# Performance work log

Hardware: AMD Instinct MI355X
Metric: run time of the kernel (lower is better)

Reference implementation:

```python
import jax, jax.numpy as jnp
import numpy as np

CODEBOOK = 512
EMB_DIM = 64
COMMITMENT_COST = 0.25


def setup_inputs() -> dict:
    key = jax.random.key(0)
    k1, k2 = jax.random.split(key)
    inputs = jax.random.normal(k1, (32, EMB_DIM, 64, 64), dtype=jnp.float32)
    # nn.Embedding weight initialized uniform(-1/code_book_dim, 1/code_book_dim)
    embedding = jax.random.uniform(
        k2, (CODEBOOK, EMB_DIM), dtype=jnp.float32,
        minval=-1.0 / CODEBOOK, maxval=1.0 / CODEBOOK)
    return {"inputs": inputs, "embedding": embedding}


def reference(inputs, embedding):
    B, C, H, W = inputs.shape          # C == embedding_dim
    D = embedding.shape[1]
    x = jnp.transpose(inputs, (0, 2, 3, 1))      # [B,H,W,D] (permute(0,2,3,1))
    flat = x.reshape(-1, D)                       # [N,D]
    x2 = jnp.sum(flat * flat, axis=1, keepdims=True)          # [N,1]
    e2 = jnp.sum(embedding * embedding, axis=1)[None, :]       # [1,K]
    xe = flat @ embedding.T                                    # [N,K]
    distances = (x2 - 2.0 * xe + e2) / D                       # [N,K]
    encoding_indices = jnp.argmin(distances, axis=1)           # [N]
    quantized = embedding[encoding_indices].reshape(x.shape)   # [B,H,W,D]
    # MSE losses with detach semantics
    e_latent_loss = jnp.mean((jax.lax.stop_gradient(quantized) - x) ** 2)
    q_latent_loss = jnp.mean((quantized - jax.lax.stop_gradient(x)) ** 2)
    loss = q_latent_loss + COMMITMENT_COST * e_latent_loss
    # straight-through estimator (module default training=True)
    quantized_st = x + jax.lax.stop_gradient(quantized - x)
    out = jnp.transpose(quantized_st, (0, 3, 1, 2))            # back to NCHW
    indices = encoding_indices.reshape(B, -1)                  # [B, H*W]
    return loss, out, indices
```

## Files before the change

kernel.cpp:

```cpp
#include <hip/hip_runtime.h>


#define KCODE 512
#define EMB   64
#define HWSZ  4096
#define NPOS  131072
#define DELTA 2.5e-4f

typedef short short8  __attribute__((ext_vector_type(8)));
typedef float float4v __attribute__((ext_vector_type(4)));


__device__ __forceinline__ float np_sumsq64(const float* a) {
    #pragma clang fp contract(off)
    {
        float r0 = a[0] * a[0], r1 = a[1] * a[1], r2 = a[2] * a[2], r3 = a[3] * a[3];
        float r4 = a[4] * a[4], r5 = a[5] * a[5], r6 = a[6] * a[6], r7 = a[7] * a[7];
        for (int i = 8; i < 64; i += 8) {
            r0 += a[i + 0] * a[i + 0];
            r1 += a[i + 1] * a[i + 1];
            r2 += a[i + 2] * a[i + 2];
            r3 += a[i + 3] * a[i + 3];
            r4 += a[i + 4] * a[i + 4];
            r5 += a[i + 5] * a[i + 5];
            r6 += a[i + 6] * a[i + 6];
            r7 += a[i + 7] * a[i + 7];
        }
        return ((r0 + r1) + (r2 + r3)) + ((r4 + r5) + (r6 + r7));
    }
}

__device__ __forceinline__ float exact_u(const float* x, float x2,
                                         const float* ek, float e2k) {
    float t0 = 0.f, t1 = 0.f, t2 = 0.f, t3 = 0.f;
    #pragma unroll
    for (int c = 0; c < EMB; c += 4) {
        t0 = fmaf(x[c + 0], ek[c + 0], t0);
        t1 = fmaf(x[c + 1], ek[c + 1], t1);
        t2 = fmaf(x[c + 2], ek[c + 2], t2);
        t3 = fmaf(x[c + 3], ek[c + 3], t3);
    }
    float xe  = (t0 + t1) + (t2 + t3);
    float tmp = x2 - 2.0f * xe;
    return tmp + e2k;
}

__device__ __forceinline__ unsigned short bf16rne(float f) {
    unsigned u = __float_as_uint(f);
    unsigned r = (u + 0x7FFFu + ((u >> 16) & 1u)) >> 16;
    return (unsigned short)r;
}
__device__ __forceinline__ float bf16tof(unsigned short h) {
    return __uint_as_float((unsigned)h << 16);
}

#define INS(M1, I1, M2, I2, M3, v, i)                      \
    {                                                      \
        bool lt1 = (v) < (M1), lt2 = (v) < (M2), lt3 = (v) < (M3); \
        (M3) = lt2 ? (M2) : (lt3 ? (v) : (M3));            \
        (I2) = lt1 ? (I1) : (lt2 ? (i) : (I2));            \
        (M2) = lt1 ? (M1) : (lt2 ? (v) : (M2));            \
        (M1) = lt1 ? (v) : (M1);                           \
        (I1) = lt1 ? (i) : (I1);                           \
    }

__global__ void vq_prep(const float* __restrict__ emb, float* __restrict__ ws) {
    int f = blockIdx.x * blockDim.x + threadIdx.x;
    if (f == 0) { ((unsigned*)ws)[0] = 0u; ((unsigned*)ws)[1] = 0u; }
    if (f < KCODE) ws[520 + f] = np_sumsq64(emb + f * EMB);
    short8* bfrag = (short8*)(ws + 1032);
    int l = f & 63;
    int c = (f >> 6) & 1;
    int t = f >> 7;
    int code  = t * 16 + (l & 15);
    int dbase = 32 * c + ((l >> 4) & 3) * 8;
    const float* e = emb + code * EMB + dbase;
    short8 h, lo;
    #pragma unroll
    for (int j = 0; j < 8; ++j) {
        float v = e[j];
        unsigned short hb = bf16rne(v);
        float hf = bf16tof(hb);
        unsigned short lb = bf16rne(v - hf);
        h[j]  = (short)hb;
        lo[j] = (short)lb;
    }
    bfrag[t * 256 + c * 128 + 0 * 64 + l] = h;
    bfrag[t * 256 + c * 128 + 1 * 64 + l] = lo;
}

__global__ __launch_bounds__(256, 3) void vq_screen(
        const float*  __restrict__ in,
        const float*  __restrict__ e2np,
        const short8* __restrict__ bfrag,
        float*        __restrict__ out_idx,
        unsigned*     __restrict__ fullCnt,
        unsigned*     __restrict__ fullList,
        int fullCap) {
    const int tid  = threadIdx.x;
    const int wave = tid >> 6;
    const int lane = tid & 63;
    const int lg   = lane >> 4;
    const int lc   = lane & 15;
    const int wavePos = blockIdx.x * 128 + wave * 32;

    short8 fH[2][2], fL[2][2];
    #pragma unroll
    for (int pt = 0; pt < 2; ++pt) {
        int pos = wavePos + pt * 16 + lc;
        int b   = pos >> 12;
        int hw  = pos & (HWSZ - 1);
        const float* xb = in + ((size_t)b << 18) + hw;
        #pragma unroll
        for (int c = 0; c < 2; ++c) {
            short8 h, lo;
            #pragma unroll
            for (int j = 0; j < 8; ++j) {
                int d = 32 * c + lg * 8 + j;
                float g = -2.0f * xb[(size_t)d << 12];
                unsigned short hb = bf16rne(g);
                float hf = bf16tof(hb);
                unsigned short lb = bf16rne(g - hf);
                h[j]  = (short)hb;
                lo[j] = (short)lb;
            }
            fH[pt][c] = h;
            fL[pt][c] = lo;
        }
    }

    float m1[2][4], m2[2][4], m3[2][4];
    int   i1[2][4], i2[2][4];
    #pragma unroll
    for (int pt = 0; pt < 2; ++pt)
        #pragma unroll
        for (int r = 0; r < 4; ++r) {
            m1[pt][r] = 3.4e38f; m2[pt][r] = 3.4e38f; m3[pt][r] = 3.4e38f;
            i1[pt][r] = 0;       i2[pt][r] = 0;
        }

    short8 ceh0 = bfrag[lane],       cel0 = bfrag[64 + lane];
    short8 ceh1 = bfrag[128 + lane], cel1 = bfrag[192 + lane];
    float  ce2  = e2np[lc];
    #pragma unroll 2
    for (int t = 0; t < 32; ++t) {
        short8 neh0, nel0, neh1, nel1;
        float  ne2 = 0.0f;
        if (t < 31) {
            const short8* nb = bfrag + (t + 1) * 256;
            neh0 = nb[lane];       nel0 = nb[64 + lane];
            neh1 = nb[128 + lane]; nel1 = nb[192 + lane];
            ne2  = e2np[(t + 1) * 16 + lc];
        }
        const int kf = t * 16 + lc;
        #pragma unroll
        for (int pt = 0; pt < 2; ++pt) {
            float4v aH = {ce2, ce2, ce2, ce2};
            float4v aM = {0.f, 0.f, 0.f, 0.f};
            float4v aL = {0.f, 0.f, 0.f, 0.f};
            aH = __builtin_amdgcn_mfma_f32_16x16x32_bf16(fH[pt][0], ceh0, aH, 0, 0, 0);
            aM = __builtin_amdgcn_mfma_f32_16x16x32_bf16(fH[pt][0], cel0, aM, 0, 0, 0);
            aL = __builtin_amdgcn_mfma_f32_16x16x32_bf16(fL[pt][0], ceh0, aL, 0, 0, 0);
            aH = __builtin_amdgcn_mfma_f32_16x16x32_bf16(fH[pt][1], ceh1, aH, 0, 0, 0);
            aM = __builtin_amdgcn_mfma_f32_16x16x32_bf16(fH[pt][1], cel1, aM, 0, 0, 0);
            aL = __builtin_amdgcn_mfma_f32_16x16x32_bf16(fL[pt][1], ceh1, aL, 0, 0, 0);
            #pragma unroll
            for (int r = 0; r < 4; ++r) {
                float sv = (aH[r] + aM[r]) + aL[r];
                INS(m1[pt][r], i1[pt][r], m2[pt][r], i2[pt][r], m3[pt][r], sv, kf);
            }
        }
        ceh0 = neh0; cel0 = nel0; ceh1 = neh1; cel1 = nel1; ce2 = ne2;
    }

    #pragma unroll
    for (int pt = 0; pt < 2; ++pt) {
        #pragma unroll
        for (int r = 0; r < 4; ++r) {
            float M1 = m1[pt][r], M2 = m2[pt][r], M3 = m3[pt][r];
            int   I1 = i1[pt][r], I2 = i2[pt][r];
            #pragma unroll
            for (int d = 1; d <= 8; d <<= 1) {
                float pm1 = __shfl_xor(M1, d, 64);
                int   pi1 = __shfl_xor(I1, d, 64);
                float pm2 = __shfl_xor(M2, d, 64);
                int   pi2 = __shfl_xor(I2, d, 64);
                float pm3 = __shfl_xor(M3, d, 64);
                INS(M1, I1, M2, I2, M3, pm1, pi1);
                INS(M1, I1, M2, I2, M3, pm2, pi2);
                M3 = fminf(M3, pm3);
            }
            m1[pt][r] = M1; m2[pt][r] = M2; m3[pt][r] = M3;
            i1[pt][r] = I1; i2[pt][r] = I2;
        }
    }

    if (lc == 0) {
        #pragma unroll
        for (int pt = 0; pt < 2; ++pt) {
            #pragma unroll
            for (int r = 0; r < 4; ++r) {
                int p  = wavePos + pt * 16 + lg * 4 + r;
                int g2 = (m2[pt][r] - m1[pt][r] <= DELTA) ? 1 : 0;
                int g3 = (m3[pt][r] - m1[pt][r] <= DELTA) ? 1 : 0;
                int packed = i1[pt][r] | (i2[pt][r] << 9) | (g2 << 18) | (g3 << 19);
                out_idx[p] = (float)packed;
                if (g3) {
                    unsigned slot = atomicAdd(fullCnt, 1u);
                    if (slot < (unsigned)fullCap) fullList[slot] = (unsigned)p;
                }
            }
        }
    }
}

__global__ __launch_bounds__(64) void vq_full(
        const float* __restrict__ in, const float* __restrict__ emb,
        const float* __restrict__ e2np, const unsigned* __restrict__ fullCnt,
        const unsigned* __restrict__ fullList, int fullCap,
        float* __restrict__ out_idx) {
    __shared__ float xbuf[EMB];
    const int lane = threadIdx.x;
    unsigned cnt = *fullCnt;
    if (cnt > (unsigned)fullCap) cnt = (unsigned)fullCap;

    for (unsigned idx = blockIdx.x; idx < cnt; idx += gridDim.x) {
        const int n  = (int)fullList[idx];
        const int b  = n >> 12;
        const int hw = n & (HWSZ - 1);
        xbuf[lane] = in[((size_t)b << 18) + ((size_t)lane << 12) + hw];
        __syncthreads();

        float x2;
        {
            #pragma clang fp contract(off)
            float r0 = xbuf[0] * xbuf[0], r1 = xbuf[1] * xbuf[1];
            float r2 = xbuf[2] * xbuf[2], r3 = xbuf[3] * xbuf[3];
            float r4 = xbuf[4] * xbuf[4], r5 = xbuf[5] * xbuf[5];
            float r6 = xbuf[6] * xbuf[6], r7 = xbuf[7] * xbuf[7];
            #pragma unroll 1
            for (int i = 8; i < EMB; i += 8) {
                r0 += xbuf[i + 0] * xbuf[i + 0];
                r1 += xbuf[i + 1] * xbuf[i + 1];
                r2 += xbuf[i + 2] * xbuf[i + 2];
                r3 += xbuf[i + 3] * xbuf[i + 3];
                r4 += xbuf[i + 4] * xbuf[i + 4];
                r5 += xbuf[i + 5] * xbuf[i + 5];
                r6 += xbuf[i + 6] * xbuf[i + 6];
                r7 += xbuf[i + 7] * xbuf[i + 7];
            }
            x2 = ((r0 + r1) + (r2 + r3)) + ((r4 + r5) + (r6 + r7));
        }

        float bu = 3.4e38f;
        int   bk = 0x7fffffff;
        #pragma unroll 1
        for (int j = 0; j < 8; ++j) {
            const int k = j * 64 + lane;
            const float* ek = emb + (size_t)k * EMB;
            float t0 = 0.f, t1 = 0.f, t2 = 0.f, t3 = 0.f;
            #pragma unroll 4
            for (int c = 0; c < EMB; c += 4) {
                t0 = fmaf(xbuf[c + 0], ek[c + 0], t0);
                t1 = fmaf(xbuf[c + 1], ek[c + 1], t1);
                t2 = fmaf(xbuf[c + 2], ek[c + 2], t2);
                t3 = fmaf(xbuf[c + 3], ek[c + 3], t3);
            }
            float xe  = (t0 + t1) + (t2 + t3);
            float tmp = x2 - 2.0f * xe;
            float u   = tmp + e2np[k];
            if (u < bu || (u == bu && k < bk)) { bu = u; bk = k; }
        }
        #pragma unroll
        for (int d = 1; d < 64; d <<= 1) {
            float ou = __shfl_xor(bu, d, 64);
            int   ok = __shfl_xor(bk, d, 64);
            if (ou < bu || (ou == bu && ok < bk)) { bu = ou; bk = ok; }
        }
        if (lane == 0) out_idx[n] = (float)bk;
        __syncthreads();
    }
}

__global__ __launch_bounds__(256) void vq_write(
        const float* __restrict__ in, const float* __restrict__ emb,
        const float* __restrict__ e2np,
        float* __restrict__ out_idx, float* __restrict__ out_q,
        float* __restrict__ partials,
        unsigned* __restrict__ ticket,
        float* __restrict__ out_loss) {
    const int tid = threadIdx.x;
    const int n   = blockIdx.x * 256 + tid;
    const int b   = n >> 12;
    const int hw  = n & (HWSZ - 1);

    const float* xp = in + ((size_t)b << 18) + hw;
    float x[EMB];
    #pragma unroll
    for (int c = 0; c < EMB; ++c) x[c] = xp[(size_t)c << 12];

    int v = (int)out_idx[n];
    int k = v & 511;
    int fl = v >> 18;
    if (fl) {
        float x2 = np_sumsq64(x);
        if (fl & 2) {
            float bu = 3.4e38f; int bk = 0;
            for (int kk = 0; kk < KCODE; ++kk) {
                float u = exact_u(x, x2, emb + kk * EMB, e2np[kk]);
                if (u < bu) { bu = u; bk = kk; }
            }
            k = bk;
        } else {
            int ia = v & 511, ib = (v >> 9) & 511;
            float u1 = exact_u(x, x2, emb + ia * EMB, e2np[ia]);
            float u2 = exact_u(x, x2, emb + ib * EMB, e2np[ib]);
            k = (u1 < u2) ? ia : (u2 < u1 ? ib : (ia < ib ? ia : ib));
        }
    }
    out_idx[n] = (float)k;

    const float4* qk = (const float4*)(emb + (size_t)k * EMB);
    float* op = out_q + ((size_t)b << 18) + hw;
    float s = 0.0f;
    #pragma unroll
    for (int c4 = 0; c4 < EMB / 4; ++c4) {
        float4 q = qk[c4];
        float d0 = q.x - x[c4 * 4 + 0];
        float d1 = q.y - x[c4 * 4 + 1];
        float d2 = q.z - x[c4 * 4 + 2];
        float d3 = q.w - x[c4 * 4 + 3];
        s = fmaf(d0, d0, s); s = fmaf(d1, d1, s);
        s = fmaf(d2, d2, s); s = fmaf(d3, d3, s);
        op[(size_t)(c4 * 4 + 0) << 12] = q.x;
        op[(size_t)(c4 * 4 + 1) << 12] = q.y;
        op[(size_t)(c4 * 4 + 2) << 12] = q.z;
        op[(size_t)(c4 * 4 + 3) << 12] = q.w;
    }

    #pragma unroll
    for (int off = 32; off > 0; off >>= 1)
        s += __shfl_down(s, off, 64);
    __shared__ float red[4];
    const int wave = tid >> 6;
    const int lane = tid & 63;
    if (lane == 0) red[wave] = s;
    __syncthreads();
    if (tid == 0) {
        partials[blockIdx.x] = (red[0] + red[1]) + (red[2] + red[3]);
        __threadfence();
        unsigned tk = atomicAdd(ticket, 1u);
        if (tk == 511u) {
            __threadfence();
            float a0 = 0.f, a1 = 0.f, a2 = 0.f, a3 = 0.f;
            float a4 = 0.f, a5 = 0.f, a6 = 0.f, a7 = 0.f;
            for (int i = 0; i < 512; i += 8) {
                a0 += partials[i + 0]; a1 += partials[i + 1];
                a2 += partials[i + 2]; a3 += partials[i + 3];
                a4 += partials[i + 4]; a5 += partials[i + 5];
                a6 += partials[i + 6]; a7 += partials[i + 7];
            }
            float tot = ((a0 + a1) + (a2 + a3)) + ((a4 + a5) + (a6 + a7));
            out_loss[0] = 1.25f * tot * (1.0f / ((float)NPOS * (float)EMB));
        }
    }
}

extern "C" void kernel_launch(void* const* d_in, const int* in_sizes, int n_in,
                              void* d_out, int out_size, void* d_ws, size_t ws_size,
                              hipStream_t stream) {
    const float* in  = (const float*)d_in[0];
    const float* emb = (const float*)d_in[1];
    float* ws  = (float*)d_ws;
    float* out = (float*)d_out;

    float*    out_loss = out;
    float*    out_q    = out + 1;
    float*    out_idx  = out + 1 + (size_t)NPOS * EMB;
    unsigned* fullCnt  = (unsigned*)ws;
    unsigned* ticket   = (unsigned*)ws + 1;
    float*    partials = ws + 8;
    float*    e2np     = ws + 520;
    short8*   bfrag    = (short8*)(ws + 1032);
    unsigned* fullList = (unsigned*)(ws + 33800);

    long avail = (long)(ws_size / 4) - 33800;
    int  fullCap = avail > 0 ? (avail > 1024 ? 1024 : (int)avail) : 0;

    vq_prep<<<16, 256, 0, stream>>>(emb, ws);
    vq_screen<<<NPOS / 128, 256, 0, stream>>>(in, e2np, bfrag, out_idx,
                                              fullCnt, fullList, fullCap);
    vq_full<<<256, 64, 0, stream>>>(in, emb, e2np, fullCnt, fullList, fullCap,
                                    out_idx);
    vq_write<<<NPOS / 256, 256, 0, stream>>>(in, emb, e2np, out_idx, out_q,
                                             partials, ticket, out_loss);
}
```

Baseline: 183.6 us.

## Compute loss from screen distances and skip input reload in write kernel

The loss is now computed inside the screening kernel from the squared norm of x plus the minimum screened distance, and accumulated with a global atomic and a ticket. This lets the write kernel skip reloading all 64 input channels for most positions. Near-tie positions with two candidates are resolved in a separate list-driven kernel, vq_res2, and full-search candidates keep their own list. The loss now comes from bf16-split approximate distances rather than exact squared differences, which may change precision. It also adds float atomics on one address, which make the summation order nondeterministic.

Result: slower. 222.0 us (+20.9%).

```diff
diff --git a/kernel.cpp b/kernel.cpp
--- a/kernel.cpp
+++ b/kernel.cpp
@@ -66,7 +66,12 @@
 
 __global__ void vq_prep(const float* __restrict__ emb, float* __restrict__ ws) {
     int f = blockIdx.x * blockDim.x + threadIdx.x;
-    if (f == 0) { ((unsigned*)ws)[0] = 0u; ((unsigned*)ws)[1] = 0u; }
+    if (f == 0) {
+        ((unsigned*)ws)[0] = 0u;
+        ((unsigned*)ws)[1] = 0u;
+        ((unsigned*)ws)[2] = 0u;
+        ws[3] = 0.0f;
+    }
     if (f < KCODE) ws[520 + f] = np_sumsq64(emb + f * EMB);
     short8* bfrag = (short8*)(ws + 1032);
     int l = f & 63;
@@ -94,9 +99,14 @@
         const float*  __restrict__ e2np,
         const short8* __restrict__ bfrag,
         float*        __restrict__ out_idx,
-        unsigned*     __restrict__ fullCnt,
-        unsigned*     __restrict__ fullList,
-        int fullCap) {
+        unsigned*     __restrict__ g3cnt,
+        unsigned*     __restrict__ g2cnt,
+        float*        __restrict__ loss_acc,
+        unsigned*     __restrict__ ticket,
+        unsigned*     __restrict__ g3list,
+        unsigned*     __restrict__ g2list,
+        int g3cap, int g2cap,
+        float*        __restrict__ out_loss) {
     const int tid  = threadIdx.x;
     const int wave = tid >> 6;
     const int lane = tid & 63;
@@ -105,12 +115,14 @@
     const int wavePos = blockIdx.x * 128 + wave * 32;
 
     short8 fH[2][2], fL[2][2];
+    float  x2p[2];
     #pragma unroll
     for (int pt = 0; pt < 2; ++pt) {
         int pos = wavePos + pt * 16 + lc;
         int b   = pos >> 12;
         int hw  = pos & (HWSZ - 1);
         const float* xb = in + ((size_t)b << 18) + hw;
+        float sq = 0.0f;
         #pragma unroll
         for (int c = 0; c < 2; ++c) {
             short8 h, lo;
@@ -118,6 +130,7 @@
             for (int j = 0; j < 8; ++j) {
                 int d = 32 * c + lg * 8 + j;
                 float g = -2.0f * xb[(size_t)d << 12];
+                sq = fmaf(g, g, sq);
                 unsigned short hb = bf16rne(g);
                 float hf = bf16tof(hb);
                 unsigned short lb = bf16rne(g - hf);
@@ -127,6 +140,14 @@
             fH[pt][c] = h;
             fL[pt][c] = lo;
         }
+        x2p[pt] = sq;
+    }
+    #pragma unroll
+    for (int pt = 0; pt < 2; ++pt) {
+        float v2 = x2p[pt];
+        v2 += __shfl_xor(v2, 16, 64);
+        v2 += __shfl_xor(v2, 32, 64);
+        x2p[pt] = v2 * 0.25f;
     }
 
     float m1[2][4], m2[2][4], m3[2][4];
@@ -195,37 +216,98 @@
         }
     }
 
+    float lossl = 0.0f;
+    #pragma unroll
+    for (int pt = 0; pt < 2; ++pt) {
+        #pragma unroll
+        for (int r = 0; r < 4; ++r) {
+            float xx = __shfl(x2p[pt], lg * 4 + r, 64);
+            lossl += xx + m1[pt][r];
+        }
+    }
+    if (lc != 0) lossl = 0.0f;
+
     if (lc == 0) {
         #pragma unroll
         for (int pt = 0; pt < 2; ++pt) {
             #pragma unroll
             for (int r = 0; r < 4; ++r) {
                 int p  = wavePos + pt * 16 + lg * 4 + r;
-                int g2 = (m2[pt][r] - m1[pt][r] <= DELTA) ? 1 : 0;
-                int g3 = (m3[pt][r] - m1[pt][r] <= DELTA) ? 1 : 0;
-                int packed = i1[pt][r] | (i2[pt][r] << 9) | (g2 << 18) | (g3 << 19);
-                out_idx[p] = (float)packed;
-                if (g3) {
-                    unsigned slot = atomicAdd(fullCnt, 1u);
-                    if (slot < (unsigned)fullCap) fullList[slot] = (unsigned)p;
+                bool g2 = (m2[pt][r] - m1[pt][r] <= DELTA);
+                bool g3 = (m3[pt][r] - m1[pt][r] <= DELTA);
+                if (!g2) {
+                    out_idx[p] = (float)i1[pt][r];
+                } else {
+                    int packed = i1[pt][r] | (i2[pt][r] << 9)
+                               | (1 << 18) | (g3 ? (1 << 19) : 0);
+                    out_idx[p] = (float)packed;
+                    if (g3) {
+                        unsigned s = atomicAdd(g3cnt, 1u);
+                        if (s < (unsigned)g3cap) g3list[s] = (unsigned)p;
+                    } else {
+                        unsigned s = atomicAdd(g2cnt, 1u);
+                        if (s < (unsigned)g2cap) g2list[s] = (unsigned)p;
+                    }
                 }
             }
         }
+    }
+
+    #pragma unroll
+    for (int off = 32; off > 0; off >>= 1)
+        lossl += __shfl_down(lossl, off, 64);
+    __shared__ float red[4];
+    if (lane == 0) red[wave] = lossl;
+    __syncthreads();
+    if (tid == 0) {
+        atomicAdd(loss_acc, (red[0] + red[1]) + (red[2] + red[3]));
+        __threadfence();
+        unsigned tk = atomicAdd(ticket, 1u);
+        if (tk == (unsigned)(gridDim.x - 1)) {
+            float tot = atomicAdd(loss_acc, 0.0f);
+            out_loss[0] = 1.25f * tot * (1.0f / ((float)NPOS * (float)EMB));
+        }
+    }
+}
+
+__global__ __launch_bounds__(64) void vq_res2(
+        const float* __restrict__ in, const float* __restrict__ emb,
+        const float* __restrict__ e2np, const unsigned* __restrict__ g2cnt,
+        const unsigned* __restrict__ g2list, int g2cap,
+        float* __restrict__ out_idx) {
+    unsigned cnt = *g2cnt;
+    if (cnt > (unsigned)g2cap) cnt = (unsigned)g2cap;
+    for (unsigned idx = blockIdx.x * 64 + threadIdx.x; idx < cnt;
+         idx += gridDim.x * 64) {
+        const int n  = (int)g2list[idx];
+        const int b  = n >> 12;
+        const int hw = n & (HWSZ - 1);
+        const float* xp = in + ((size_t)b << 18) + hw;
+        float x[EMB];
+        #pragma unroll
+        for (int c = 0; c < EMB; ++c) x[c] = xp[(size_t)c << 12];
+        const float x2 = np_sumsq64(x);
+        const int v  = (int)out_idx[n];
+        const int ia = v & 511, ib = (v >> 9) & 511;
+        float u1 = exact_u(x, x2, emb + (size_t)ia * EMB, e2np[ia]);
+        float u2 = exact_u(x, x2, emb + (size_t)ib * EMB, e2np[ib]);
+        int kk = (u1 < u2) ? ia : (u2 < u1 ? ib : (ia < ib ? ia : ib));
+        out_idx[n] = (float)kk;
     }
 }
 
 __global__ __launch_bounds__(64) void vq_full(
         const float* __restrict__ in, const float* __restrict__ emb,
-        const float* __restrict__ e2np, const unsigned* __restrict__ fullCnt,
-        const unsigned* __restrict__ fullList, int fullCap,
+        const float* __restrict__ e2np, const unsigned* __restrict__ g3cnt,
+        const unsigned* __restrict__ g3list, int g3cap,
         float* __restrict__ out_idx) {
     __shared__ float xbuf[EMB];
     const int lane = threadIdx.x;
-    unsigned cnt = *fullCnt;
-    if (cnt > (unsigned)fullCap) cnt = (unsigned)fullCap;
+    unsigned cnt = *g3cnt;
+    if (cnt > (unsigned)g3cap) cnt = (unsigned)g3cap;
 
     for (unsigned idx = blockIdx.x; idx < cnt; idx += gridDim.x) {
-        const int n  = (int)fullList[idx];
+        const int n  = (int)g3list[idx];
         const int b  = n >> 12;
         const int hw = n & (HWSZ - 1);
         xbuf[lane] = in[((size_t)b << 18) + ((size_t)lane << 12) + hw];
@@ -285,84 +367,45 @@
 __global__ __launch_bounds__(256) void vq_write(
         const float* __restrict__ in, const float* __restrict__ emb,
         const float* __restrict__ e2np,
-        float* __restrict__ out_idx, float* __restrict__ out_q,
-        float* __restrict__ partials,
-        unsigned* __restrict__ ticket,
-        float* __restrict__ out_loss) {
+        float* __restrict__ out_idx, float* __restrict__ out_q) {
     const int tid = threadIdx.x;
     const int n   = blockIdx.x * 256 + tid;
     const int b   = n >> 12;
     const int hw  = n & (HWSZ - 1);
 
-    const float* xp = in + ((size_t)b << 18) + hw;
-    float x[EMB];
-    #pragma unroll
-    for (int c = 0; c < EMB; ++c) x[c] = xp[(size_t)c << 12];
-
-    int v = (int)out_idx[n];
-    int k = v & 511;
-    int fl = v >> 18;
-    if (fl) {
+    int v  = (int)out_idx[n];
+    int kk = v & 511;
+    if (v >> 18) {
+        const float* xp = in + ((size_t)b << 18) + hw;
+        float x[EMB];
+        #pragma unroll
+        for (int c = 0; c < EMB; ++c) x[c] = xp[(size_t)c << 12];
         float x2 = np_sumsq64(x);
-        if (fl & 2) {
+        if (v & (1 << 19)) {
             float bu = 3.4e38f; int bk = 0;
-            for (int kk = 0; kk < KCODE; ++kk) {
-                float u = exact_u(x, x2, emb + kk * EMB, e2np[kk]);
-                if (u < bu) { bu = u; bk = kk; }
-            }
-            k = bk;
+            for (int k = 0; k < KCODE; ++k) {
+                float u = exact_u(x, x2, emb + k * EMB, e2np[k]);
+                if (u < bu) { bu = u; bk = k; }
+            }
+            kk = bk;
         } else {
             int ia = v & 511, ib = (v >> 9) & 511;
             float u1 = exact_u(x, x2, emb + ia * EMB, e2np[ia]);
             float u2 = exact_u(x, x2, emb + ib * EMB, e2np[ib]);
-            k = (u1 < u2) ? ia : (u2 < u1 ? ib : (ia < ib ? ia : ib));
-        }
-    }
-    out_idx[n] = (float)k;
-
-    const float4* qk = (const float4*)(emb + (size_t)k * EMB);
+            kk = (u1 < u2) ? ia : (u2 < u1 ? ib : (ia < ib ? ia : ib));
+        }
+        out_idx[n] = (float)kk;
+    }
+
+    const float4* qk = (const float4*)(emb + (size_t)kk * EMB);
     float* op = out_q + ((size_t)b << 18) + hw;
-    float s = 0.0f;
     #pragma unroll
     for (int c4 = 0; c4 < EMB / 4; ++c4) {
         float4 q = qk[c4];
-        float d0 = q.x - x[c4 * 4 + 0];
-        float d1 = q.y - x[c4 * 4 + 1];
-        float d2 = q.z - x[c4 * 4 + 2];
-        float d3 = q.w - x[c4 * 4 + 3];
-        s = fmaf(d0, d0, s); s = fmaf(d1, d1, s);
-        s = fmaf(d2, d2, s); s = fmaf(d3, d3, s);
         op[(size_t)(c4 * 4 + 0) << 12] = q.x;
         op[(size_t)(c4 * 4 + 1) << 12] = q.y;
         op[(size_t)(c4 * 4 + 2) << 12] = q.z;
         op[(size_t)(c4 * 4 + 3) << 12] = q.w;
-    }
-
-    #pragma unroll
-    for (int off = 32; off > 0; off >>= 1)
-        s += __shfl_down(s, off, 64);
-    __shared__ float red[4];
-    const int wave = tid >> 6;
-    const int lane = tid & 63;
-    if (lane == 0) red[wave] = s;
-    __syncthreads();
-    if (tid == 0) {
-        partials[blockIdx.x] = (red[0] + red[1]) + (red[2] + red[3]);
-        __threadfence();
-        unsigned tk = atomicAdd(ticket, 1u);
-        if (tk == 511u) {
-            __threadfence();
-            float a0 = 0.f, a1 = 0.f, a2 = 0.f, a3 = 0.f;
-            float a4 = 0.f, a5 = 0.f, a6 = 0.f, a7 = 0.f;
-            for (int i = 0; i < 512; i += 8) {
-                a0 += partials[i + 0]; a1 += partials[i + 1];
-                a2 += partials[i + 2]; a3 += partials[i + 3];
-                a4 += partials[i + 4]; a5 += partials[i + 5];
-                a6 += partials[i + 6]; a7 += partials[i + 7];
-            }
-            float tot = ((a0 + a1) + (a2 + a3)) + ((a4 + a5) + (a6 + a7));
-            out_loss[0] = 1.25f * tot * (1.0f / ((float)NPOS * (float)EMB));
-        }
     }
 }
 
@@ -377,21 +420,27 @@
     float*    out_loss = out;
     float*    out_q    = out + 1;
     float*    out_idx  = out + 1 + (size_t)NPOS * EMB;
-    unsigned* fullCnt  = (unsigned*)ws;
+    unsigned* g3cnt    = (unsigned*)ws + 0;
     unsigned* ticket   = (unsigned*)ws + 1;
-    float*    partials = ws + 8;
+    unsigned* g2cnt    = (unsigned*)ws + 2;
+    float*    loss_acc = ws + 3;
     float*    e2np     = ws + 520;
     short8*   bfrag    = (short8*)(ws + 1032);
-    unsigned* fullList = (unsigned*)(ws + 33800);
-
-    long avail = (long)(ws_size / 4) - 33800;
-    int  fullCap = avail > 0 ? (avail > 1024 ? 1024 : (int)avail) : 0;
+    unsigned* g3list   = (unsigned*)(ws + 33800);
+    unsigned* g2list   = (unsigned*)(ws + 34824);
+
+    const int g3cap = 1024;
+    long avail = (long)(ws_size / 4) - 34824;
+    int  g2cap = avail > 0 ? (avail > 8192 ? 8192 : (int)avail) : 0;
 
     vq_prep<<<16, 256, 0, stream>>>(emb, ws);
     vq_screen<<<NPOS / 128, 256, 0, stream>>>(in, e2np, bfrag, out_idx,
-                                              fullCnt, fullList, fullCap);
-    vq_full<<<256, 64, 0, stream>>>(in, emb, e2np, fullCnt, fullList, fullCap,
+                                              g3cnt, g2cnt, loss_acc, ticket,
+                                              g3list, g2list, g3cap, g2cap,
+                                              out_loss);
+    vq_res2<<<128, 64, 0, stream>>>(in, emb, e2np, g2cnt, g2list, g2cap,
                                     out_idx);
-    vq_write<<<NPOS / 256, 256, 0, stream>>>(in, emb, e2np, out_idx, out_q,
-                                             partials, ticket, out_loss);
-}
+    vq_full<<<256, 64, 0, stream>>>(in, emb, e2np, g3cnt, g3list, g3cap,
+                                    out_idx);
+    vq_write<<<NPOS / 256, 256, 0, stream>>>(in, emb, e2np, out_idx, out_q);
+}
```
